# Performance work log

Hardware: AMD Instinct MI355X
Metric: run time of the kernel (lower is better)

Reference implementation:

```python
import jax, jax.numpy as jnp
import numpy as np


def setup_inputs() -> dict:
    key = jax.random.key(0)
    k1, k2, k3, k4 = jax.random.split(key, 4)
    B, C, W, H = 4, 64, 512, 512
    cF = jax.random.normal(k1, (B, C, W, H), dtype=jnp.float32)
    sF = jax.random.uniform(k2, (B, C, W, H), dtype=jnp.float32)
    alpha = jnp.array([0.6], dtype=jnp.float32)
    # style eigenvalues: strictly > 1e-5 so k_s == C (full rank), matching the
    # module's k_s = sum(s_e > 1e-5) slicing when the style SVD is well-conditioned
    s_e = jax.random.uniform(k3, (B, C), dtype=jnp.float32) + 0.5
    s_v = jax.random.normal(k4, (B, C, C), dtype=jnp.float32)
    return {"cF": cF, "sF": sF, "alpha": alpha, "s_e": s_e, "s_v": s_v}


def reference(cF, sF, alpha, s_e, s_v):
    B, C, W, H = cF.shape
    N = W * H
    cf = cF.reshape(B, C, N)            # [B, C, WH]
    sf = sF.reshape(B, C, -1)           # [B, C, W1H1]

    # ---- whiten content ----
    c_mean = jnp.mean(cf, axis=2, keepdims=True)
    cfc = cf - c_mean                   # centered content
    # covariance + I  (I shift => all eigenvalues >= 1, so k_c == C)
    cov = jnp.einsum('bcn,bdn->bcd', cfc, cfc) / (N - 1) + jnp.eye(C, dtype=cf.dtype)
    _, c_e, c_vh = jnp.linalg.svd(cov, full_matrices=False)
    c_d = c_e ** -0.5
    # original: step2 = (Vh @ diag(c_d)) @ Vh^T  -> fuse diag as column scale
    step2 = jnp.einsum('bij,bj,blj->bil', c_vh, c_d, c_vh)
    whiten_cF = jnp.einsum('bcd,bdn->bcn', step2, cfc)

    # ---- color with style stats ----
    s_mean = jnp.mean(sf, axis=2, keepdims=True)
    s_d = s_e ** 0.5                    # k_s == C by construction of s_e
    colorM = jnp.einsum('bij,bj,blj->bil', s_v, s_d, s_v)
    target = jnp.einsum('bcd,bdn->bcn', colorM, whiten_cF) + s_mean

    a = alpha.reshape(())
    csF = a * target + (1.0 - a) * cf
    return csF.reshape(B, C, W, H).astype(jnp.float32)
```

## Files before the change

### kernel.cpp

```cpp
#include <hip/hip_runtime.h>
#include <math.h>

#define WS_G 0
#define WS_SC 16384
#define WS_SS 16640
#define WS_T 16896
#define WS_BIAS 33280
#define WS_ZERO_COUNT 16896

__device__ __forceinline__ float waveRed(float v) {
#pragma unroll
    for (int o = 32; o > 0; o >>= 1) v += __shfl_down(v, o, 64);
    return v;
}

__global__ void zero_kernel(float* __restrict__ ws, int n) {
    int i = blockIdx.x * 256 + threadIdx.x;
    if (i < n) ws[i] = 0.f;
}

__global__ __launch_bounds__(256) void sum_kernel(const float* __restrict__ x,
                                                  float* __restrict__ sums, int N) {
    const int ch = blockIdx.x >> 3;
    const int part = blockIdx.x & 7;
    const int seg = N >> 3;
    const float4* p = reinterpret_cast<const float4*>(x + (size_t)ch * N + (size_t)part * seg);
    const int nf4 = seg >> 2;
    float acc = 0.f;
    for (int i = threadIdx.x; i < nf4; i += 256) {
        float4 v = p[i];
        acc += (v.x + v.y) + (v.z + v.w);
    }
    acc = waveRed(acc);
    __shared__ float red[4];
    if ((threadIdx.x & 63) == 0) red[threadIdx.x >> 6] = acc;
    __syncthreads();
    if (threadIdx.x == 0) atomicAdd(&sums[ch], (red[0] + red[1]) + (red[2] + red[3]));
}

#define GSTR 129
__global__ __launch_bounds__(256) void gram_kernel(const float* __restrict__ cF,
                                                   float* __restrict__ G,
                                                   float* __restrict__ Sc, int N) {
    __shared__ float tile[64 * GSTR];
    const int b = blockIdx.x >> 7;
    const int part = blockIdx.x & 127;
    const float* base = cF + (size_t)b * 64 * N + (size_t)part * (N >> 7);
    const int t = threadIdx.x;
    const int c0 = (t >> 4) << 2;
    const int d0 = (t & 15) << 2;
    float acc[4][4];
#pragma unroll
    for (int i = 0; i < 4; ++i)
#pragma unroll
        for (int j = 0; j < 4; ++j) acc[i][j] = 0.f;
    float rowsum = 0.f;
    for (int sub = 0; sub < 16; ++sub) {
        const float* gsrc = base + sub * 128;
#pragma unroll
        for (int i = 0; i < 8; ++i) {
            int f = t + 256 * i;
            int row = f >> 5, col4 = f & 31;
            float4 v = *reinterpret_cast<const float4*>(gsrc + (size_t)row * N + col4 * 4);
            float* d = &tile[row * GSTR + col4 * 4];
            d[0] = v.x; d[1] = v.y; d[2] = v.z; d[3] = v.w;
        }
        __syncthreads();
        if (t < 64) {
            const float* tr = &tile[t * GSTR];
#pragma unroll 8
            for (int x = 0; x < 128; ++x) rowsum += tr[x];
        }
        const float* ta = &tile[c0 * GSTR];
        const float* tb = &tile[d0 * GSTR];
#pragma unroll 4
        for (int x = 0; x < 128; ++x) {
            float a0 = ta[0 * GSTR + x], a1 = ta[1 * GSTR + x];
            float a2 = ta[2 * GSTR + x], a3 = ta[3 * GSTR + x];
            float b0 = tb[0 * GSTR + x], b1 = tb[1 * GSTR + x];
            float b2 = tb[2 * GSTR + x], b3 = tb[3 * GSTR + x];
            acc[0][0] += a0 * b0; acc[0][1] += a0 * b1; acc[0][2] += a0 * b2; acc[0][3] += a0 * b3;
            acc[1][0] += a1 * b0; acc[1][1] += a1 * b1; acc[1][2] += a1 * b2; acc[1][3] += a1 * b3;
            acc[2][0] += a2 * b0; acc[2][1] += a2 * b1; acc[2][2] += a2 * b2; acc[2][3] += a2 * b3;
            acc[3][0] += a3 * b0; acc[3][1] += a3 * b1; acc[3][2] += a3 * b2; acc[3][3] += a3 * b3;
        }
        __syncthreads();
    }
    float* Gb = G + b * 4096;
#pragma unroll
    for (int i = 0; i < 4; ++i)
#pragma unroll
        for (int j = 0; j < 4; ++j) atomicAdd(&Gb[(c0 + i) * 64 + d0 + j], acc[i][j]);
    if (t < 64) atomicAdd(&Sc[b * 64 + t], rowsum);
}

#define SSTR 68

__device__ __forceinline__ void matmul44(float* __restrict__ D, const float* __restrict__ A,
                                         const float* __restrict__ Bm, int i0, int j0) {
    float acc[4][4];
#pragma unroll
    for (int i = 0; i < 4; ++i)
#pragma unroll
        for (int j = 0; j < 4; ++j) acc[i][j] = 0.f;
    for (int k = 0; k < 64; ++k) {
        float4 bv = *reinterpret_cast<const float4*>(&Bm[k * SSTR + j0]);
        float a0 = A[(i0 + 0) * SSTR + k];
        float a1 = A[(i0 + 1) * SSTR + k];
        float a2 = A[(i0 + 2) * SSTR + k];
        float a3 = A[(i0 + 3) * SSTR + k];
        acc[0][0] += a0 * bv.x; acc[0][1] += a0 * bv.y; acc[0][2] += a0 * bv.z; acc[0][3] += a0 * bv.w;
        acc[1][0] += a1 * bv.x; acc[1][1] += a1 * bv.y; acc[1][2] += a1 * bv.z; acc[1][3] += a1 * bv.w;
        acc[2][0] += a2 * bv.x; acc[2][1] += a2 * bv.y; acc[2][2] += a2 * bv.z; acc[2][3] += a2 * bv.w;
        acc[3][0] += a3 * bv.x; acc[3][1] += a3 * bv.y; acc[3][2] += a3 * bv.z; acc[3][3] += a3 * bv.w;
    }
#pragma unroll
    for (int i = 0; i < 4; ++i)
#pragma unroll
        for (int j = 0; j < 4; ++j) D[(i0 + i) * SSTR + j0 + j] = acc[i][j];
}

__global__ __launch_bounds__(256) void solve_kernel(const float* __restrict__ G,
                                                    const float* __restrict__ Sc,
                                                    const float* __restrict__ Ss,
                                                    const float* __restrict__ alphap,
                                                    const float* __restrict__ s_e,
                                                    const float* __restrict__ s_v,
                                                    float* __restrict__ Tg,
                                                    float* __restrict__ biasg, int N) {
    __shared__ __align__(16) float Abuf[64 * SSTR];
    __shared__ __align__(16) float Ybuf[64 * SSTR];
    __shared__ __align__(16) float Tbuf[64 * SSTR];
    __shared__ __align__(16) float Wb[64 * 20];
    __shared__ float sdv[64], mcv[64], msv[64];
    __shared__ float redv;
    const int b = blockIdx.x, t = threadIdx.x;
    const int i0 = (t >> 4) << 2, j0 = (t & 15) << 2;
    const float invN = 1.f / (float)N;
    const float invNm1 = 1.f / (float)(N - 1);
    if (t < 64) {
        mcv[t] = Sc[b * 64 + t] * invN;
        msv[t] = Ss[b * 64 + t] * invN;
        sdv[t] = sqrtf(s_e[b * 64 + t]);
    }
    __syncthreads();
#pragma unroll
    for (int i = 0; i < 4; ++i) {
        float mi = mcv[i0 + i];
#pragma unroll
        for (int j = 0; j < 4; ++j) {
            float g = G[b * 4096 + (i0 + i) * 64 + j0 + j];
            float cov = (g - mi * mcv[j0 + j] * (float)N) * invNm1 + (((i0 + i) == (j0 + j)) ? 1.f : 0.f);
            Abuf[(i0 + i) * SSTR + j0 + j] = cov;
        }
    }
    __syncthreads();
    if (t < 64) {
        float d = waveRed(Abuf[t * SSTR + t]);
        if (t == 0) redv = d * (1.f / 64.f);
    }
    __syncthreads();
    const float s = redv;
    const float inv_s = 1.f / s;
#pragma unroll
    for (int i = 0; i < 4; ++i)
#pragma unroll
        for (int j = 0; j < 4; ++j) {
            Abuf[(i0 + i) * SSTR + j0 + j] *= inv_s;
            Ybuf[(i0 + i) * SSTR + j0 + j] = ((i0 + i) == (j0 + j)) ? 1.f : 0.f;
        }
    __syncthreads();
    const int kr = t >> 2;
    const int cw = (t & 3) << 2;
    for (int it = 0; it < 3; ++it) {
        matmul44(Tbuf, Ybuf, Ybuf, i0, j0);
        __syncthreads();
        for (int lb = 0; lb < 4; ++lb) {
            const int cb = lb << 4;
            float w0 = 0.f, w1 = 0.f, w2 = 0.f, w3 = 0.f;
            for (int j = 0; j < 64; ++j) {
                float a = Abuf[kr * SSTR + j];
                float4 tv = *reinterpret_cast<const float4*>(&Tbuf[j * SSTR + cb + cw]);
                w0 += a * tv.x; w1 += a * tv.y; w2 += a * tv.z; w3 += a * tv.w;
            }
            Wb[kr * 20 + cw + 0] = ((kr == cb + cw + 0) ? 1.5f : 0.f) - 0.5f * w0;
            Wb[kr * 20 + cw + 1] = ((kr == cb + cw + 1) ? 1.5f : 0.f) - 0.5f * w1;
            Wb[kr * 20 + cw + 2] = ((kr == cb + cw + 2) ? 1.5f : 0.f) - 0.5f * w2;
            Wb[kr * 20 + cw + 3] = ((kr == cb + cw + 3) ? 1.5f : 0.f) - 0.5f * w3;
            __syncthreads();
            float y0 = 0.f, y1 = 0.f, y2 = 0.f, y3 = 0.f;
            for (int k = 0; k < 64; ++k) {
                float a = Ybuf[kr * SSTR + k];
                float4 wv = *reinterpret_cast<const float4*>(&Wb[k * 20 + cw]);
                y0 += a * wv.x; y1 += a * wv.y; y2 += a * wv.z; y3 += a * wv.w;
            }
            Tbuf[kr * SSTR + cb + cw + 0] = y0;
            Tbuf[kr * SSTR + cb + cw + 1] = y1;
            Tbuf[kr * SSTR + cb + cw + 2] = y2;
            Tbuf[kr * SSTR + cb + cw + 3] = y3;
            __syncthreads();
        }
#pragma unroll
        for (int i = 0; i < 4; ++i)
#pragma unroll
            for (int j = 0; j < 4; ++j)
                Ybuf[(i0 + i) * SSTR + j0 + j] = Tbuf[(i0 + i) * SSTR + j0 + j];
        __syncthreads();
    }
    for (int i = 0; i < 16; ++i) {
        int idx = t + 256 * i;
        Abuf[(idx >> 6) * SSTR + (idx & 63)] = s_v[b * 4096 + idx];
    }
    __syncthreads();
    {
        float acc[4][4];
#pragma unroll
        for (int i = 0; i < 4; ++i)
#pragma unroll
            for (int j = 0; j < 4; ++j) acc[i][j] = 0.f;
        for (int k = 0; k < 64; ++k) {
            float sd = sdv[k];
            float a0 = Abuf[(i0 + 0) * SSTR + k] * sd;
            float a1 = Abuf[(i0 + 1) * SSTR + k] * sd;
            float a2 = Abuf[(i0 + 2) * SSTR + k] * sd;
            float a3 = Abuf[(i0 + 3) * SSTR + k] * sd;
            float c0v = Abuf[(j0 + 0) * SSTR + k];
            float c1v = Abuf[(j0 + 1) * SSTR + k];
            float c2v = Abuf[(j0 + 2) * SSTR + k];
            float c3v = Abuf[(j0 + 3) * SSTR + k];
            acc[0][0] += a0 * c0v; acc[0][1] += a0 * c1v; acc[0][2] += a0 * c2v; acc[0][3] += a0 * c3v;
            acc[1][0] += a1 * c0v; acc[1][1] += a1 * c1v; acc[1][2] += a1 * c2v; acc[1][3] += a1 * c3v;
            acc[2][0] += a2 * c0v; acc[2][1] += a2 * c1v; acc[2][2] += a2 * c2v; acc[2][3] += a2 * c3v;
            acc[3][0] += a3 * c0v; acc[3][1] += a3 * c1v; acc[3][2] += a3 * c2v; acc[3][3] += a3 * c3v;
        }
        __syncthreads();
#pragma unroll
        for (int i = 0; i < 4; ++i)
#pragma unroll
            for (int j = 0; j < 4; ++j) Tbuf[(i0 + i) * SSTR + j0 + j] = acc[i][j];
    }
    __syncthreads();
    matmul44(Abuf, Tbuf, Ybuf, i0, j0);
    __syncthreads();
    const float alpha_v = alphap[0];
    const float fac = alpha_v / sqrtf(s);
#pragma unroll
    for (int i = 0; i < 4; ++i)
#pragma unroll
        for (int j = 0; j < 4; ++j) {
            float m = Abuf[(i0 + i) * SSTR + j0 + j] * fac;
            if ((i0 + i) == (j0 + j)) m += 1.f - alpha_v;
            Tg[b * 4096 + (i0 + i) * 64 + j0 + j] = m;
        }
    if (t < 64) {
        float acc = 0.f;
        for (int d = 0; d < 64; ++d) acc += Abuf[t * SSTR + d] * mcv[d];
        biasg[b * 64 + t] = alpha_v * msv[t] - fac * acc;
    }
}

#define ASTR 132
__global__ __launch_bounds__(256) void apply_kernel(const float* __restrict__ cF,
                                                    const float* __restrict__ T,
                                                    const float* __restrict__ bias,
                                                    float* __restrict__ out, int N) {
    __shared__ __align__(16) float tile[64 * ASTR];
    __shared__ float Tl[64 * 65];
    __shared__ float bl[64];
    const int b = blockIdx.x >> 9;
    const int part = blockIdx.x & 511;
    const int chunk = N >> 9;
    const float* src = cF + (size_t)b * 64 * N + (size_t)part * chunk;
    float* dst = out + (size_t)b * 64 * N + (size_t)part * chunk;
    const int t = threadIdx.x;
    for (int i = 0; i < 16; ++i) {
        int idx = t + 256 * i;
        Tl[(idx >> 6) * 65 + (idx & 63)] = T[b * 4096 + idx];
    }
    if (t < 64) bl[t] = bias[b * 64 + t];
    const int x0 = (t & 7) * 4;
    const int cA = (t >> 3) * 2;
    for (int sub = 0; sub < 4; ++sub) {
        __syncthreads();
        const float* gsrc = src + sub * 128;
#pragma unroll
        for (int i = 0; i < 8; ++i) {
            int f = t + 256 * i;
            int row = f >> 5, col4 = f & 31;
            *reinterpret_cast<float4*>(&tile[row * ASTR + col4 * 4]) =
                *reinterpret_cast<const float4*>(gsrc + (size_t)row * N + col4 * 4);
        }
        __syncthreads();
        float b0 = bl[cA], b1 = bl[cA + 1];
        float4 acc0[4], acc1[4];
#pragma unroll
        for (int g = 0; g < 4; ++g) {
            acc0[g] = make_float4(b0, b0, b0, b0);
            acc1[g] = make_float4(b1, b1, b1, b1);
        }
        const float* t0 = &Tl[cA * 65];
        const float* t1 = &Tl[(cA + 1) * 65];
#pragma unroll 2
        for (int k = 0; k < 64; ++k) {
            float a0 = t0[k], a1 = t1[k];
            const float* trow = &tile[k * ASTR + x0];
#pragma unroll
            for (int g = 0; g < 4; ++g) {
                float4 v = *reinterpret_cast<const float4*>(trow + 32 * g);
                acc0[g].x += a0 * v.x; acc0[g].y += a0 * v.y; acc0[g].z += a0 * v.z; acc0[g].w += a0 * v.w;
                acc1[g].x += a1 * v.x; acc1[g].y += a1 * v.y; acc1[g].z += a1 * v.z; acc1[g].w += a1 * v.w;
            }
        }
        float* d0 = dst + (size_t)cA * N + sub * 128 + x0;
        float* d1 = dst + (size_t)(cA + 1) * N + sub * 128 + x0;
#pragma unroll
        for (int g = 0; g < 4; ++g) {
            *reinterpret_cast<float4*>(d0 + 32 * g) = acc0[g];
            *reinterpret_cast<float4*>(d1 + 32 * g) = acc1[g];
        }
    }
}

extern "C" void kernel_launch(void* const* d_in, const int* in_sizes, int n_in,
                              void* d_out, int out_size, void* d_ws, size_t ws_size,
                              hipStream_t stream) {
    const float* cF = (const float*)d_in[0];
    const float* sF = (const float*)d_in[1];
    const float* alpha = (const float*)d_in[2];
    const float* s_e = (const float*)d_in[3];
    const float* s_v = (const float*)d_in[4];
    float* out = (float*)d_out;
    float* ws = (float*)d_ws;
    const int B = 4, C = 64;
    const int N = in_sizes[0] / (B * C);
    float* G = ws + WS_G;
    float* Sc = ws + WS_SC;
    float* Ss = ws + WS_SS;
    float* T = ws + WS_T;
    float* bias = ws + WS_BIAS;
    hipLaunchKernelGGL(zero_kernel, dim3(66), dim3(256), 0, stream, ws, WS_ZERO_COUNT);
    hipLaunchKernelGGL(sum_kernel, dim3(B * C * 8), dim3(256), 0, stream, sF, Ss, N);
    hipLaunchKernelGGL(gram_kernel, dim3(B * 128), dim3(256), 0, stream, cF, G, Sc, N);
    hipLaunchKernelGGL(solve_kernel, dim3(B), dim3(256), 0, stream, G, Sc, Ss, alpha, s_e, s_v, T, bias, N);
    hipLaunchKernelGGL(apply_kernel, dim3(B * 512), dim3(256), 0, stream, cF, T, bias, out, N);
}
```

Measured before the change: 872.8 us.

## Compute content Gram matrix with split-bf16 MFMA and register prefetch

The scalar FP32 outer-product Gram kernel is replaced by bf16 MFMA 32x32x16 instructions. Each float is split into hi and lo bf16 parts and three products are accumulated to approximate FP32 precision. The next tile is prefetched into registers while the current one is packed into a slab layout in LDS, and row sums are computed from registers with shuffles. This targets the ALU-bound Gram pass, at some cost in precision compared with true FP32 and extra packing work.

```diff
diff --git a/kernel.cpp b/kernel.cpp
--- a/kernel.cpp
+++ b/kernel.cpp
@@ -7,6 +7,9 @@
 #define WS_T 16896
 #define WS_BIAS 33280
 #define WS_ZERO_COUNT 16896
+
+typedef __attribute__((ext_vector_type(8))) short bf16x8;
+typedef __attribute__((ext_vector_type(16))) float f32x16;
 
 __device__ __forceinline__ float waveRed(float v) {
 #pragma unroll
@@ -38,60 +41,106 @@
     if (threadIdx.x == 0) atomicAdd(&sums[ch], (red[0] + red[1]) + (red[2] + red[3]));
 }
 
-#define GSTR 129
+#define GR_SLAB 1040
+#define GR_PLANE 16640
 __global__ __launch_bounds__(256) void gram_kernel(const float* __restrict__ cF,
                                                    float* __restrict__ G,
                                                    float* __restrict__ Sc, int N) {
-    __shared__ float tile[64 * GSTR];
+    __shared__ __align__(16) char smem[2 * GR_PLANE];
     const int b = blockIdx.x >> 7;
     const int part = blockIdx.x & 127;
     const float* base = cF + (size_t)b * 64 * N + (size_t)part * (N >> 7);
     const int t = threadIdx.x;
-    const int c0 = (t >> 4) << 2;
-    const int d0 = (t & 15) << 2;
-    float acc[4][4];
-#pragma unroll
-    for (int i = 0; i < 4; ++i)
-#pragma unroll
-        for (int j = 0; j < 4; ++j) acc[i][j] = 0.f;
-    float rowsum = 0.f;
-    for (int sub = 0; sub < 16; ++sub) {
-        const float* gsrc = base + sub * 128;
+    const int wid = t >> 6;
+    const int lane = t & 63;
+    const int I = (wid >> 1) << 5;
+    const int Jt = (wid & 1) << 5;
+    const bool diag = (I == Jt);
+    const int rA = I + (lane & 31);
+    const int rB = Jt + (lane & 31);
+    const int sl = lane >> 5;
+
+    f32x16 acc = {};
+    float rs[8];
+#pragma unroll
+    for (int i = 0; i < 8; ++i) rs[i] = 0.f;
+
+    float4 v[8];
+#pragma unroll
+    for (int i = 0; i < 8; ++i) {
+        int f = t + 256 * i;
+        v[i] = *reinterpret_cast<const float4*>(base + (size_t)(f >> 5) * N + (f & 31) * 4);
+    }
+
+    for (int c = 0; c < 16; ++c) {
+        uint2 hw[8], lw[8];
+#pragma unroll
+        for (int i = 0; i < 8; ++i) {
+            float4 x = v[i];
+            rs[i] += (x.x + x.y) + (x.z + x.w);
+            unsigned bx = __float_as_uint(x.x), by = __float_as_uint(x.y);
+            unsigned bz = __float_as_uint(x.z), bw = __float_as_uint(x.w);
+            float lx = x.x - __uint_as_float(bx & 0xffff0000u);
+            float ly = x.y - __uint_as_float(by & 0xffff0000u);
+            float lz = x.z - __uint_as_float(bz & 0xffff0000u);
+            float lwv = x.w - __uint_as_float(bw & 0xffff0000u);
+            hw[i] = make_uint2((bx >> 16) | (by & 0xffff0000u),
+                               (bz >> 16) | (bw & 0xffff0000u));
+            lw[i] = make_uint2((__float_as_uint(lx) >> 16) | (__float_as_uint(ly) & 0xffff0000u),
+                               (__float_as_uint(lz) >> 16) | (__float_as_uint(lwv) & 0xffff0000u));
+        }
+        __syncthreads();
 #pragma unroll
         for (int i = 0; i < 8; ++i) {
             int f = t + 256 * i;
             int row = f >> 5, col4 = f & 31;
-            float4 v = *reinterpret_cast<const float4*>(gsrc + (size_t)row * N + col4 * 4);
-            float* d = &tile[row * GSTR + col4 * 4];
-            d[0] = v.x; d[1] = v.y; d[2] = v.z; d[3] = v.w;
-        }
-        __syncthreads();
-        if (t < 64) {
-            const float* tr = &tile[t * GSTR];
-#pragma unroll 8
-            for (int x = 0; x < 128; ++x) rowsum += tr[x];
-        }
-        const float* ta = &tile[c0 * GSTR];
-        const float* tb = &tile[d0 * GSTR];
-#pragma unroll 4
-        for (int x = 0; x < 128; ++x) {
-            float a0 = ta[0 * GSTR + x], a1 = ta[1 * GSTR + x];
-            float a2 = ta[2 * GSTR + x], a3 = ta[3 * GSTR + x];
-            float b0 = tb[0 * GSTR + x], b1 = tb[1 * GSTR + x];
-            float b2 = tb[2 * GSTR + x], b3 = tb[3 * GSTR + x];
-            acc[0][0] += a0 * b0; acc[0][1] += a0 * b1; acc[0][2] += a0 * b2; acc[0][3] += a0 * b3;
-            acc[1][0] += a1 * b0; acc[1][1] += a1 * b1; acc[1][2] += a1 * b2; acc[1][3] += a1 * b3;
-            acc[2][0] += a2 * b0; acc[2][1] += a2 * b1; acc[2][2] += a2 * b2; acc[2][3] += a2 * b3;
-            acc[3][0] += a3 * b0; acc[3][1] += a3 * b1; acc[3][2] += a3 * b2; acc[3][3] += a3 * b3;
-        }
-        __syncthreads();
-    }
+            char* dst = smem + (col4 >> 1) * GR_SLAB + row * 16 + ((col4 & 1) << 3);
+            *reinterpret_cast<uint2*>(dst) = hw[i];
+            *reinterpret_cast<uint2*>(dst + GR_PLANE) = lw[i];
+        }
+        if (c < 15) {
+            const float* gn = base + (c + 1) * 128;
+#pragma unroll
+            for (int i = 0; i < 8; ++i) {
+                int f = t + 256 * i;
+                v[i] = *reinterpret_cast<const float4*>(gn + (size_t)(f >> 5) * N + (f & 31) * 4);
+            }
+        }
+        __syncthreads();
+#pragma unroll
+        for (int kc = 0; kc < 8; ++kc) {
+            const char* sb = smem + (2 * kc + sl) * GR_SLAB;
+            bf16x8 ahi = *reinterpret_cast<const bf16x8*>(sb + rA * 16);
+            bf16x8 alo = *reinterpret_cast<const bf16x8*>(sb + GR_PLANE + rA * 16);
+            bf16x8 bhi, blo;
+            if (diag) {
+                bhi = ahi; blo = alo;
+            } else {
+                bhi = *reinterpret_cast<const bf16x8*>(sb + rB * 16);
+                blo = *reinterpret_cast<const bf16x8*>(sb + GR_PLANE + rB * 16);
+            }
+            acc = __builtin_amdgcn_mfma_f32_32x32x16_bf16(ahi, bhi, acc, 0, 0, 0);
+            acc = __builtin_amdgcn_mfma_f32_32x32x16_bf16(ahi, blo, acc, 0, 0, 0);
+            acc = __builtin_amdgcn_mfma_f32_32x32x16_bf16(alo, bhi, acc, 0, 0, 0);
+        }
+        __syncthreads();
+    }
+
     float* Gb = G + b * 4096;
 #pragma unroll
-    for (int i = 0; i < 4; ++i)
-#pragma unroll
-        for (int j = 0; j < 4; ++j) atomicAdd(&Gb[(c0 + i) * 64 + d0 + j], acc[i][j]);
-    if (t < 64) atomicAdd(&Sc[b * 64 + t], rowsum);
+    for (int r = 0; r < 16; ++r) {
+        int m = (r & 3) + 8 * (r >> 2) + 4 * (lane >> 5);
+        int n = lane & 31;
+        atomicAdd(&Gb[(I + m) * 64 + (Jt + n)], acc[r]);
+    }
+    const int baseRow = t >> 5;
+#pragma unroll
+    for (int i = 0; i < 8; ++i) {
+        float s = rs[i];
+#pragma unroll
+        for (int o = 16; o > 0; o >>= 1) s += __shfl_xor(s, o);
+        if ((lane & 31) == 0) atomicAdd(&Sc[b * 64 + baseRow + 8 * i], s);
+    }
 }
 
 #define SSTR 68
```

Measured after the change: 757.3 us. 1.15x faster.
